# Optimization experiments

Measured on AMD Instinct MI355X. Metric: run time of the kernel, lower is better.

## Reference

```python
import jax, jax.numpy as jnp
import numpy as np

NEG_SLOPE = 0.2


def gat_layer(x, src, dst, W, a_src, a_dst, bias, num_nodes, concat):
    """PyG-style GATConv (eval mode, self-loops already included in src/dst).
    x: [N, F_in]; W: [F_in, H*C]; a_src, a_dst: [H, C]; bias: [H*C] or [C].
    """
    H, C = a_src.shape
    h = (x @ W).reshape(num_nodes, H, C)                    # [N,H,C]
    alpha_s = jnp.einsum('nhc,hc->nh', h, a_src)            # [N,H]
    alpha_d = jnp.einsum('nhc,hc->nh', h, a_dst)            # [N,H]
    e = alpha_s[src] + alpha_d[dst]                         # [E,H]
    e = jnp.where(e > 0, e, NEG_SLOPE * e)                  # LeakyReLU(0.2)
    # segment softmax over destination nodes (numerically stable)
    m = jax.ops.segment_max(e, dst, num_segments=num_nodes)  # [N,H]
    m = jnp.where(jnp.isfinite(m), m, 0.0)
    ex = jnp.exp(e - m[dst])                                # [E,H]
    s = jax.ops.segment_sum(ex, dst, num_segments=num_nodes)  # [N,H]
    alpha = ex / (s[dst] + 1e-16)                           # [E,H]
    msg = h[src] * alpha[:, :, None]                        # [E,H,C]
    out = jax.ops.segment_sum(msg, dst, num_segments=num_nodes)  # [N,H,C]
    if concat:
        out = out.reshape(num_nodes, H * C)
    else:
        out = out.mean(axis=1)
    return out + bias


def _forward(x, edge_index, W1, a_src1, a_dst1, b1, W2, a_src2, a_dst2, b2):
    N = x.shape[0]
    loops = jnp.arange(N, dtype=edge_index.dtype)
    src = jnp.concatenate([edge_index[0], loops])
    dst = jnp.concatenate([edge_index[1], loops])
    h = gat_layer(x, src, dst, W1, a_src1, a_dst1, b1, N, concat=True)
    h = jax.nn.relu(h)  # dropout inactive in eval
    h = gat_layer(h, src, dst, W2, a_src2, a_dst2, b2, N, concat=False)
    return jax.nn.log_softmax(h, axis=1)


def setup_inputs() -> dict:
    key = jax.random.key(0)
    ks = jax.random.split(key, 10)
    N, E, F_in, Hid, H1, F_out = 100000, 1600000, 128, 64, 2, 7
    x = jax.random.normal(ks[0], (N, F_in), dtype=jnp.float32)
    edge_index = jax.random.randint(ks[1], (2, E), 0, N, dtype=jnp.int64)
    s1 = 1.0 / np.sqrt(F_in)
    W1 = jax.random.uniform(ks[2], (F_in, H1 * Hid), jnp.float32, -s1, s1)
    a_src1 = jax.random.uniform(ks[3], (H1, Hid), jnp.float32, -s1, s1)
    a_dst1 = jax.random.uniform(ks[4], (H1, Hid), jnp.float32, -s1, s1)
    b1 = jnp.zeros((H1 * Hid,), jnp.float32)
    s2 = 1.0 / np.sqrt(H1 * Hid)
    W2 = jax.random.uniform(ks[5], (H1 * Hid, F_out), jnp.float32, -s2, s2)
    a_src2 = jax.random.uniform(ks[6], (1, F_out), jnp.float32, -s2, s2)
    a_dst2 = jax.random.uniform(ks[7], (1, F_out), jnp.float32, -s2, s2)
    b2 = jnp.zeros((F_out,), jnp.float32)
    return {"x": x, "edge_index": edge_index, "W1": W1, "a_src1": a_src1,
            "a_dst1": a_dst1, "b1": b1, "W2": W2, "a_src2": a_src2,
            "a_dst2": a_dst2, "b2": b2}


def reference(x, edge_index, W1, a_src1, a_dst1, b1, W2, a_src2, a_dst2, b2):
    return _forward(x, edge_index, W1, a_src1, a_dst1, b1, W2, a_src2, a_dst2, b2)
```

## Files before the change

kernel.cpp:

```cpp
#include <hip/hip_runtime.h>
#include <hip/hip_bf16.h>

#define F_IN 128
#define HC   128
#define C1   64
#define F_OUT 7
#define H2S  8
#define BSH  9
#define BSZ  512
#define BINCH 8192
#define BCAP 12288

typedef __attribute__((ext_vector_type(8))) short short8;
typedef __attribute__((ext_vector_type(4))) float f32x4;
typedef __attribute__((ext_vector_type(2))) float f32x2;

__device__ __forceinline__ ushort f2bf(float f) {
    uint u = __builtin_bit_cast(uint, f);
    u = (u + 0x7FFFu + ((u >> 16) & 1u)) >> 16;
    return (ushort)u;
}

__global__ __launch_bounds__(256) void k_bincvt(
    const int* __restrict__ ei, int E, int Etot, int NBIN,
    int* __restrict__ bcnt, uint* __restrict__ binned,
    const float* __restrict__ W1, ushort* __restrict__ Wsw,
    const float* __restrict__ W2, const float* __restrict__ b1,
    float* __restrict__ W2p, float* __restrict__ b1p)
{
    int b = blockIdx.x, t = threadIdx.x;
    if (b < NBIN) {
        __shared__ int hist[256];
        __shared__ int base[256];
        hist[t] = 0;
        __syncthreads();
        long c0 = (long)b * BINCH;
#pragma unroll
        for (int i = 0; i < BINCH / 256; ++i) {
            long e = c0 + t + i * 256;
            if (e < Etot) {
                int d = (e < E) ? ei[E + e] : (int)(e - E);
                atomicAdd(&hist[d >> BSH], 1);
            }
        }
        __syncthreads();
        base[t] = t * BCAP + ((hist[t] > 0) ? atomicAdd(&bcnt[t], hist[t]) : 0);
        __syncthreads();
#pragma unroll
        for (int i = 0; i < BINCH / 256; ++i) {
            long e = c0 + t + i * 256;
            if (e < Etot) {
                int s, d;
                if (e < E) { s = ei[e]; d = ei[E + e]; } else { s = (int)(e - E); d = s; }
                int bkt = d >> BSH;
                int pos = atomicAdd(&base[bkt], 1);
                if (pos < (bkt + 1) * BCAP)
                    binned[pos] = ((uint)s << BSH) | (uint)(d & (BSZ - 1));
            }
        }
    } else if (b < NBIN + 64) {
        int i = (b - NBIN) * 256 + t;
        int k = i >> 7, n = i & 127;
        float v = W1[k * HC + n];
        int idx = n * 128 + (((k & ~7) ^ ((n & 7) << 3)) | (k & 7));
        Wsw[idx] = f2bf(v);
    } else {
        for (int i = t; i < 128 * F_OUT; i += 256) {
            int p = i / F_OUT, o = i - p * F_OUT;
            int c = 16 * (p & 7) + (p >> 3);
            W2p[i] = W2[c * F_OUT + o];
        }
        if (t < 128) b1p[t] = b1[16 * (t & 7) + (t >> 3)];
    }
}

__global__ __launch_bounds__(256) void k_fillgemm(
    const uint* __restrict__ binned, const int* __restrict__ bcnt,
    int* __restrict__ rowptr, int* __restrict__ csr,
    const float* __restrict__ x, const ushort* __restrict__ Wsw,
    const float* __restrict__ a_src, const float* __restrict__ a_dst,
    unsigned char* __restrict__ h1p, float* __restrict__ as1, float* __restrict__ ad1,
    int N, int NB)
{
    __shared__ __align__(16) char smem[128 * 128 * 2];
    const int t = threadIdx.x;

    if ((int)blockIdx.x < NB) {
        int* deg = (int*)smem;
        int* cur = deg + BSZ;
        int* sc  = cur + BSZ;
        int b = blockIdx.x;
        int cv = (t < NB) ? min(bcnt[t], BCAP) : 0;
        sc[t] = cv;
        __syncthreads();
        for (int off = 1; off < 256; off <<= 1) {
            int u = (t >= off) ? sc[t - off] : 0;
            __syncthreads();
            sc[t] += u;
            __syncthreads();
        }
        int total = sc[255];
        int s0 = (b > 0) ? sc[b - 1] : 0;
        int cntb = min(bcnt[b], BCAP);
        __syncthreads();

        int n0 = b << BSH;
        int nn = N - n0; if (nn > BSZ) nn = BSZ;
        deg[t] = 0; deg[t + 256] = 0;
        __syncthreads();
        const uint* bb = binned + (size_t)b * BCAP;
        for (int i = t; i < cntb; i += 256)
            atomicAdd(&deg[bb[i] & (BSZ - 1)], 1);
        __syncthreads();
        int d0 = deg[2 * t], d1 = deg[2 * t + 1];
        int ts = d0 + d1;
        sc[t] = ts;
        __syncthreads();
        for (int off = 1; off < 256; off <<= 1) {
            int u = (t >= off) ? sc[t - off] : 0;
            __syncthreads();
            sc[t] += u;
            __syncthreads();
        }
        int ex = sc[t] - ts + s0;
        if (2 * t < nn)     { rowptr[n0 + 2 * t]     = ex;      cur[2 * t]     = ex; }
        if (2 * t + 1 < nn) { rowptr[n0 + 2 * t + 1] = ex + d0; cur[2 * t + 1] = ex + d0; }
        __syncthreads();
        for (int i = t; i < cntb; i += 256) {
            uint en = bb[i];
            int pos = atomicAdd(&cur[en & (BSZ - 1)], 1);
            csr[pos] = (int)(en >> BSH);
        }
        if (b == 0 && t == 0) rowptr[N] = total;
    } else {
        ushort* Bs = (ushort*)smem;
        const int w = t >> 6, l = t & 63;
        const int lr = l & 15, hi = l >> 4;
        const int n0 = (blockIdx.x - NB) * 64;

        {
            const uint4* src = (const uint4*)Wsw;
            uint4* dst = (uint4*)Bs;
#pragma unroll
            for (int it = 0; it < 8; ++it) dst[t + it * 256] = src[t + it * 256];
        }
        __syncthreads();

        f32x4 acc[8];
#pragma unroll
        for (int j = 0; j < 8; ++j) acc[j] = (f32x4){0.f, 0.f, 0.f, 0.f};

        int arow = n0 + w * 16 + lr;
        if (arow >= N) arow = N - 1;
        const float* aptr = x + (size_t)arow * F_IN + hi * 8;

#pragma unroll
        for (int kt = 0; kt < 4; ++kt) {
            float4 f0 = *(const float4*)(aptr + kt * 32);
            float4 f1 = *(const float4*)(aptr + kt * 32 + 4);
            short8 a;
            a[0] = (short)f2bf(f0.x); a[1] = (short)f2bf(f0.y);
            a[2] = (short)f2bf(f0.z); a[3] = (short)f2bf(f0.w);
            a[4] = (short)f2bf(f1.x); a[5] = (short)f2bf(f1.y);
            a[6] = (short)f2bf(f1.z); a[7] = (short)f2bf(f1.w);
#pragma unroll
            for (int j = 0; j < 8; ++j) {
                int rn = 16 * j + lr;
                int kidx = (kt * 32 + hi * 8) ^ ((rn & 7) << 3);
                short8 b = *(const short8*)(Bs + rn * 128 + kidx);
                acc[j] = __builtin_amdgcn_mfma_f32_16x16x32_bf16(a, b, acc[j], 0, 0, 0);
            }
        }

        float as_[8], ad_[8];
#pragma unroll
        for (int j = 0; j < 8; ++j) {
            int hd = j >> 2;
            int c = 16 * (j & 3) + lr;
            as_[j] = a_src[hd * C1 + c];
            ad_[j] = a_dst[hd * C1 + c];
        }
#pragma unroll
        for (int i = 0; i < 4; ++i) {
            int r = n0 + w * 16 + hi * 4 + i;
            float ps0 = 0, ps1 = 0, pd0 = 0, pd1 = 0;
#pragma unroll
            for (int j = 0; j < 4; ++j) { ps0 += acc[j][i] * as_[j]; pd0 += acc[j][i] * ad_[j]; }
#pragma unroll
            for (int j = 4; j < 8; ++j) { ps1 += acc[j][i] * as_[j]; pd1 += acc[j][i] * ad_[j]; }
#pragma unroll
            for (int off = 1; off <= 8; off <<= 1) {
                ps0 += __shfl_xor(ps0, off, 64);
                ps1 += __shfl_xor(ps1, off, 64);
                pd0 += __shfl_xor(pd0, off, 64);
                pd1 += __shfl_xor(pd1, off, 64);
            }
            if (r < N) {
                int lo = 0, hi2 = 0;
                lo  = __builtin_amdgcn_cvt_pk_fp8_f32(acc[0][i], acc[1][i], lo,  false);
                lo  = __builtin_amdgcn_cvt_pk_fp8_f32(acc[2][i], acc[3][i], lo,  true);
                hi2 = __builtin_amdgcn_cvt_pk_fp8_f32(acc[4][i], acc[5][i], hi2, false);
                hi2 = __builtin_amdgcn_cvt_pk_fp8_f32(acc[6][i], acc[7][i], hi2, true);
                *(uint2*)(h1p + (size_t)r * HC + lr * 8) = make_uint2((uint)lo, (uint)hi2);
                if (lr == 0) {
                    as1[r * 2 + 0] = ps0; as1[r * 2 + 1] = ps1;
                    ad1[r * 2 + 0] = pd0; ad1[r * 2 + 1] = pd1;
                }
            }
        }
    }
}

__global__ __launch_bounds__(256) void k_aggr1_l2(
    const int* __restrict__ rowptr, const int* __restrict__ csr_src,
    const float* __restrict__ as1, const float* __restrict__ ad1,
    const unsigned char* __restrict__ h1p, const float* __restrict__ b1p,
    const float* __restrict__ W2p, const float* __restrict__ a_src2,
    const float* __restrict__ a_dst2,
    float* __restrict__ h2p, float* __restrict__ as2, float* __restrict__ ad2,
    int N)
{
    int w = threadIdx.x >> 6, l = threadIdx.x & 63;
    int q = l >> 4, sl = l & 15;
    int n = blockIdx.x * 16 + w * 4 + q;
    if (n >= N) return;
    float2 advv = *(const float2*)&ad1[n * 2];
    int beg = rowptr[n], end = rowptr[n + 1];
    float ac[8];
#pragma unroll
    for (int c = 0; c < 8; ++c) ac[c] = 0.f;
    float s0 = 0.f, s1 = 0.f;

    int i = beg;
    for (; i + 4 <= end; i += 4) {
        int sv[4]; float2 Av[4]; uint2 Hv[4];
#pragma unroll
        for (int j = 0; j < 4; ++j) sv[j] = csr_src[i + j];
#pragma unroll
        for (int j = 0; j < 4; ++j) Av[j] = *(const float2*)&as1[sv[j] * 2];
#pragma unroll
        for (int j = 0; j < 4; ++j)
            Hv[j] = *(const uint2*)(h1p + (((size_t)(uint)sv[j]) << 7) + sl * 8);
#pragma unroll
        for (int j = 0; j < 4; ++j) {
            float a0 = Av[j].x + advv.x; a0 = a0 > 0.f ? a0 : 0.2f * a0;
            float a1 = Av[j].y + advv.y; a1 = a1 > 0.f ? a1 : 0.2f * a1;
            float e0 = __expf(a0), e1 = __expf(a1);
            s0 += e0; s1 += e1;
            f32x2 p01 = __builtin_amdgcn_cvt_pk_f32_fp8((int)Hv[j].x, false);
            f32x2 p23 = __builtin_amdgcn_cvt_pk_f32_fp8((int)Hv[j].x, true);
            f32x2 p45 = __builtin_amdgcn_cvt_pk_f32_fp8((int)Hv[j].y, false);
            f32x2 p67 = __builtin_amdgcn_cvt_pk_f32_fp8((int)Hv[j].y, true);
            ac[0] += e0 * p01[0]; ac[1] += e0 * p01[1];
            ac[2] += e0 * p23[0]; ac[3] += e0 * p23[1];
            ac[4] += e1 * p45[0]; ac[5] += e1 * p45[1];
            ac[6] += e1 * p67[0]; ac[7] += e1 * p67[1];
        }
    }
    for (; i < end; ++i) {
        int src = csr_src[i];
        float2 Av = *(const float2*)&as1[src * 2];
        uint2 hv = *(const uint2*)(h1p + (((size_t)(uint)src) << 7) + sl * 8);
        float a0 = Av.x + advv.x; a0 = a0 > 0.f ? a0 : 0.2f * a0;
        float a1 = Av.y + advv.y; a1 = a1 > 0.f ? a1 : 0.2f * a1;
        float e0 = __expf(a0), e1 = __expf(a1);
        s0 += e0; s1 += e1;
        f32x2 p01 = __builtin_amdgcn_cvt_pk_f32_fp8((int)hv.x, false);
        f32x2 p23 = __builtin_amdgcn_cvt_pk_f32_fp8((int)hv.x, true);
        f32x2 p45 = __builtin_amdgcn_cvt_pk_f32_fp8((int)hv.y, false);
        f32x2 p67 = __builtin_amdgcn_cvt_pk_f32_fp8((int)hv.y, true);
        ac[0] += e0 * p01[0]; ac[1] += e0 * p01[1];
        ac[2] += e0 * p23[0]; ac[3] += e0 * p23[1];
        ac[4] += e1 * p45[0]; ac[5] += e1 * p45[1];
        ac[6] += e1 * p67[0]; ac[7] += e1 * p67[1];
    }
    float inv0 = 1.f / (s0 + 1e-16f);
    float inv1 = 1.f / (s1 + 1e-16f);

    float4 bv0 = *(const float4*)&b1p[sl * 8];
    float4 bv1 = *(const float4*)&b1p[sl * 8 + 4];
    float v[8];
    v[0] = fmaxf(ac[0] * inv0 + bv0.x, 0.f);
    v[1] = fmaxf(ac[1] * inv0 + bv0.y, 0.f);
    v[2] = fmaxf(ac[2] * inv0 + bv0.z, 0.f);
    v[3] = fmaxf(ac[3] * inv0 + bv0.w, 0.f);
    v[4] = fmaxf(ac[4] * inv1 + bv1.x, 0.f);
    v[5] = fmaxf(ac[5] * inv1 + bv1.y, 0.f);
    v[6] = fmaxf(ac[6] * inv1 + bv1.z, 0.f);
    v[7] = fmaxf(ac[7] * inv1 + bv1.w, 0.f);

    float w2r[56];
    {
        const float4* wp = (const float4*)(W2p + sl * 56);
#pragma unroll
        for (int k = 0; k < 14; ++k) {
            float4 f = wp[k];
            w2r[4 * k + 0] = f.x; w2r[4 * k + 1] = f.y;
            w2r[4 * k + 2] = f.z; w2r[4 * k + 3] = f.w;
        }
    }
    float p[7];
#pragma unroll
    for (int j = 0; j < 7; ++j) p[j] = 0.f;
#pragma unroll
    for (int r = 0; r < 8; ++r)
#pragma unroll
        for (int j = 0; j < 7; ++j) p[j] += v[r] * w2r[r * 7 + j];
#pragma unroll
    for (int off = 1; off <= 8; off <<= 1)
#pragma unroll
        for (int j = 0; j < 7; ++j) p[j] += __shfl_xor(p[j], off, 64);

    if (sl == 0) {
        float asv = 0.f, adv2 = 0.f;
#pragma unroll
        for (int j = 0; j < 7; ++j) {
            h2p[(size_t)n * H2S + j] = p[j];
            asv += p[j] * a_src2[j];
            adv2 += p[j] * a_dst2[j];
        }
        h2p[(size_t)n * H2S + 7] = 0.f;
        as2[n] = asv; ad2[n] = adv2;
    }
}

__global__ __launch_bounds__(256) void k_aggr2ls(
    const int* __restrict__ rowptr, const int* __restrict__ csr_src,
    const float* __restrict__ as2, const float* __restrict__ ad2,
    const float* __restrict__ h2p, const float* __restrict__ b2,
    float* __restrict__ out, int N)
{
    int g = blockIdx.x * blockDim.x + threadIdx.x;
    int n = g >> 3, l = g & 7;
    if (n >= N) return;
    float adv = ad2[n];
    int beg = rowptr[n], end = rowptr[n + 1];
    float acc = 0.f, s = 0.f;
    int i = beg;
    for (; i + 4 <= end; i += 4) {
        int sv[4]; float Av[4], Hv[4];
#pragma unroll
        for (int j = 0; j < 4; ++j) sv[j] = csr_src[i + j];
#pragma unroll
        for (int j = 0; j < 4; ++j) Av[j] = as2[sv[j]];
#pragma unroll
        for (int j = 0; j < 4; ++j) Hv[j] = h2p[((size_t)(uint)sv[j]) * H2S + l];
#pragma unroll
        for (int j = 0; j < 4; ++j) {
            float a = Av[j] + adv;
            a = a > 0.f ? a : 0.2f * a;
            float e0 = __expf(a);
            s += e0;
            acc += e0 * Hv[j];
        }
    }
    for (; i < end; ++i) {
        int s0 = csr_src[i];
        float a = as2[s0] + adv;
        a = a > 0.f ? a : 0.2f * a;
        float e0 = __expf(a);
        s += e0;
        acc += e0 * h2p[((size_t)(uint)s0) * H2S + l];
    }
    float v = (l < 7) ? acc / (s + 1e-16f) + b2[l] : -1e30f;
    float m = v;
#pragma unroll
    for (int off = 1; off <= 4; off <<= 1)
        m = fmaxf(m, __shfl_xor(m, off, 8));
    float ex = (l < 7) ? __expf(v - m) : 0.f;
    float sum = ex;
#pragma unroll
    for (int off = 1; off <= 4; off <<= 1)
        sum += __shfl_xor(sum, off, 8);
    if (l < 7) out[(size_t)n * F_OUT + l] = v - m - __logf(sum);
}

extern "C" void kernel_launch(void* const* d_in, const int* in_sizes, int n_in,
                              void* d_out, int out_size, void* d_ws, size_t ws_size,
                              hipStream_t stream) {
    const float* x      = (const float*)d_in[0];
    const int*   ei     = (const int*)d_in[1];
    const float* W1     = (const float*)d_in[2];
    const float* a_src1 = (const float*)d_in[3];
    const float* a_dst1 = (const float*)d_in[4];
    const float* b1     = (const float*)d_in[5];
    const float* W2     = (const float*)d_in[6];
    const float* a_src2 = (const float*)d_in[7];
    const float* a_dst2 = (const float*)d_in[8];
    const float* b2     = (const float*)d_in[9];
    float* out = (float*)d_out;

    const int N    = in_sizes[0] / F_IN;
    const int E    = in_sizes[1] / 2;
    const int Etot = E + N;
    const int NB   = (N + BSZ - 1) >> BSH;
    const int NBIN = (Etot + BINCH - 1) / BINCH;

    char* ws = (char*)d_ws;
    size_t off = 0;
    auto A = [&](size_t bytes) -> void* {
        char* p = ws + off;
        off += (bytes + 255) & ~(size_t)255;
        return (void*)p;
    };
    ushort* Wsw    = (ushort*)A((size_t)128 * 128 * 2);
    float*  W2p    = (float*) A((size_t)128 * F_OUT * 4);
    float*  b1p    = (float*) A((size_t)128 * 4);
    unsigned char* h1p = (unsigned char*)A((size_t)N * HC);
    float*  as1    = (float*) A((size_t)N * 2 * 4);
    float*  ad1    = (float*) A((size_t)N * 2 * 4);
    int*    rowptr = (int*)   A((size_t)(N + 1) * 4);
    int*    csr    = (int*)   A((size_t)Etot * 4);
    int*    bcnt   = (int*)   A(256 * 4);
    uint*   binned = (uint*)  A((size_t)NB * BCAP * 4);
    float*  h2p    = (float*)binned;
    float*  as2    = (float*)((char*)binned + (((size_t)N * H2S * 4 + 255) & ~(size_t)255));
    float*  ad2    = (float*)((char*)as2 + (((size_t)N * 4 + 255) & ~(size_t)255));

    hipMemsetAsync(bcnt, 0, 256 * 4, stream);

    k_bincvt<<<NBIN + 65, 256, 0, stream>>>(ei, E, Etot, NBIN, bcnt, binned,
                                            W1, Wsw, W2, b1, W2p, b1p);
    k_fillgemm<<<NB + (N + 63) / 64, 256, 0, stream>>>(
        binned, bcnt, rowptr, csr,
        x, Wsw, a_src1, a_dst1, h1p, as1, ad1, N, NB);
    k_aggr1_l2<<<(N + 15) / 16, 256, 0, stream>>>(rowptr, csr, as1, ad1, h1p,
                                                  b1p, W2p, a_src2, a_dst2,
                                                  h2p, as2, ad2, N);
    k_aggr2ls<<<((size_t)N * 8 + 255) / 256, 256, 0, stream>>>(rowptr, csr, as2, ad2,
                                                               h2p, b2, out, N);
}
```

Before: 157.1 us.

## Permute h1 fp8 layout per head and halve threads in layer-2 aggregation

Changes the fp8 row layout of h1 so each lane's 8 bytes belong to a single head. Each lane in layer-1 aggregation then computes one exp and one attention load per edge instead of two, and accumulates with packed f32x2 math. W2 and b1 permutations are updated to match the new column order. Layer-2 aggregation now uses 4 lanes per node with float2 loads instead of 8 lanes, which cuts redundant csr and as2 loads and exp work but lowers thread-level parallelism.

```diff
diff --git a/kernel.cpp b/kernel.cpp
--- a/kernel.cpp
+++ b/kernel.cpp
@@ -19,6 +19,13 @@
     uint u = __builtin_bit_cast(uint, f);
     u = (u + 0x7FFFu + ((u >> 16) & 1u)) >> 16;
     return (ushort)u;
+}
+
+__device__ __forceinline__ int perm_col(int p_byte) {
+    int slp = p_byte >> 3, j = p_byte & 7;
+    int h = slp >> 3, sg = slp & 7;
+    int lr = 2 * sg + (j >> 2), jj = j & 3;
+    return 16 * (4 * h + jj) + lr;
 }
 
 __global__ __launch_bounds__(256) void k_bincvt(
@@ -67,10 +74,9 @@
     } else {
         for (int i = t; i < 128 * F_OUT; i += 256) {
             int p = i / F_OUT, o = i - p * F_OUT;
-            int c = 16 * (p & 7) + (p >> 3);
-            W2p[i] = W2[c * F_OUT + o];
-        }
-        if (t < 128) b1p[t] = b1[16 * (t & 7) + (t >> 3)];
+            W2p[i] = W2[perm_col(p) * F_OUT + o];
+        }
+        if (t < 128) b1p[t] = b1[perm_col(t)];
     }
 }
 
@@ -196,12 +202,13 @@
                 pd1 += __shfl_xor(pd1, off, 64);
             }
             if (r < N) {
-                int lo = 0, hi2 = 0;
-                lo  = __builtin_amdgcn_cvt_pk_fp8_f32(acc[0][i], acc[1][i], lo,  false);
-                lo  = __builtin_amdgcn_cvt_pk_fp8_f32(acc[2][i], acc[3][i], lo,  true);
-                hi2 = __builtin_amdgcn_cvt_pk_fp8_f32(acc[4][i], acc[5][i], hi2, false);
-                hi2 = __builtin_amdgcn_cvt_pk_fp8_f32(acc[6][i], acc[7][i], hi2, true);
-                *(uint2*)(h1p + (size_t)r * HC + lr * 8) = make_uint2((uint)lo, (uint)hi2);
+                int w0 = 0, w1 = 0;
+                w0 = __builtin_amdgcn_cvt_pk_fp8_f32(acc[0][i], acc[1][i], w0, false);
+                w0 = __builtin_amdgcn_cvt_pk_fp8_f32(acc[2][i], acc[3][i], w0, true);
+                w1 = __builtin_amdgcn_cvt_pk_fp8_f32(acc[4][i], acc[5][i], w1, false);
+                w1 = __builtin_amdgcn_cvt_pk_fp8_f32(acc[6][i], acc[7][i], w1, true);
+                *(uint*)(h1p + (size_t)r * HC + lr * 4)      = (uint)w0;
+                *(uint*)(h1p + (size_t)r * HC + 64 + lr * 4) = (uint)w1;
                 if (lr == 0) {
                     as1[r * 2 + 0] = ps0; as1[r * 2 + 1] = ps1;
                     ad1[r * 2 + 0] = pd0; ad1[r * 2 + 1] = pd1;
@@ -224,70 +231,60 @@
     int q = l >> 4, sl = l & 15;
     int n = blockIdx.x * 16 + w * 4 + q;
     if (n >= N) return;
-    float2 advv = *(const float2*)&ad1[n * 2];
+    const int h = sl >> 3;
+    const int boff = sl * 8;
+    float adv = ad1[n * 2 + h];
     int beg = rowptr[n], end = rowptr[n + 1];
-    float ac[8];
-#pragma unroll
-    for (int c = 0; c < 8; ++c) ac[c] = 0.f;
-    float s0 = 0.f, s1 = 0.f;
+    f32x2 ac01 = {0.f, 0.f}, ac23 = {0.f, 0.f}, ac45 = {0.f, 0.f}, ac67 = {0.f, 0.f};
+    float s = 0.f;
 
     int i = beg;
     for (; i + 4 <= end; i += 4) {
-        int sv[4]; float2 Av[4]; uint2 Hv[4];
+        int sv[4]; float Av[4]; uint2 Hv[4];
 #pragma unroll
         for (int j = 0; j < 4; ++j) sv[j] = csr_src[i + j];
 #pragma unroll
-        for (int j = 0; j < 4; ++j) Av[j] = *(const float2*)&as1[sv[j] * 2];
+        for (int j = 0; j < 4; ++j) Av[j] = as1[sv[j] * 2 + h];
 #pragma unroll
         for (int j = 0; j < 4; ++j)
-            Hv[j] = *(const uint2*)(h1p + (((size_t)(uint)sv[j]) << 7) + sl * 8);
+            Hv[j] = *(const uint2*)(h1p + (((size_t)(uint)sv[j]) << 7) + boff);
 #pragma unroll
         for (int j = 0; j < 4; ++j) {
-            float a0 = Av[j].x + advv.x; a0 = a0 > 0.f ? a0 : 0.2f * a0;
-            float a1 = Av[j].y + advv.y; a1 = a1 > 0.f ? a1 : 0.2f * a1;
-            float e0 = __expf(a0), e1 = __expf(a1);
-            s0 += e0; s1 += e1;
-            f32x2 p01 = __builtin_amdgcn_cvt_pk_f32_fp8((int)Hv[j].x, false);
-            f32x2 p23 = __builtin_amdgcn_cvt_pk_f32_fp8((int)Hv[j].x, true);
-            f32x2 p45 = __builtin_amdgcn_cvt_pk_f32_fp8((int)Hv[j].y, false);
-            f32x2 p67 = __builtin_amdgcn_cvt_pk_f32_fp8((int)Hv[j].y, true);
-            ac[0] += e0 * p01[0]; ac[1] += e0 * p01[1];
-            ac[2] += e0 * p23[0]; ac[3] += e0 * p23[1];
-            ac[4] += e1 * p45[0]; ac[5] += e1 * p45[1];
-            ac[6] += e1 * p67[0]; ac[7] += e1 * p67[1];
+            float a = Av[j] + adv; a = a > 0.f ? a : 0.2f * a;
+            float e = __expf(a);
+            s += e;
+            f32x2 ev = {e, e};
+            ac01 += ev * __builtin_amdgcn_cvt_pk_f32_fp8((int)Hv[j].x, false);
+            ac23 += ev * __builtin_amdgcn_cvt_pk_f32_fp8((int)Hv[j].x, true);
+            ac45 += ev * __builtin_amdgcn_cvt_pk_f32_fp8((int)Hv[j].y, false);
+            ac67 += ev * __builtin_amdgcn_cvt_pk_f32_fp8((int)Hv[j].y, true);
         }
     }
     for (; i < end; ++i) {
         int src = csr_src[i];
-        float2 Av = *(const float2*)&as1[src * 2];
-        uint2 hv = *(const uint2*)(h1p + (((size_t)(uint)src) << 7) + sl * 8);
-        float a0 = Av.x + advv.x; a0 = a0 > 0.f ? a0 : 0.2f * a0;
-        float a1 = Av.y + advv.y; a1 = a1 > 0.f ? a1 : 0.2f * a1;
-        float e0 = __expf(a0), e1 = __expf(a1);
-        s0 += e0; s1 += e1;
-        f32x2 p01 = __builtin_amdgcn_cvt_pk_f32_fp8((int)hv.x, false);
-        f32x2 p23 = __builtin_amdgcn_cvt_pk_f32_fp8((int)hv.x, true);
-        f32x2 p45 = __builtin_amdgcn_cvt_pk_f32_fp8((int)hv.y, false);
-        f32x2 p67 = __builtin_amdgcn_cvt_pk_f32_fp8((int)hv.y, true);
-        ac[0] += e0 * p01[0]; ac[1] += e0 * p01[1];
-        ac[2] += e0 * p23[0]; ac[3] += e0 * p23[1];
-        ac[4] += e1 * p45[0]; ac[5] += e1 * p45[1];
-        ac[6] += e1 * p67[0]; ac[7] += e1 * p67[1];
-    }
-    float inv0 = 1.f / (s0 + 1e-16f);
-    float inv1 = 1.f / (s1 + 1e-16f);
+        float a = as1[src * 2 + h] + adv; a = a > 0.f ? a : 0.2f * a;
+        float e = __expf(a);
+        s += e;
+        uint2 hv = *(const uint2*)(h1p + (((size_t)(uint)src) << 7) + boff);
+        f32x2 ev = {e, e};
+        ac01 += ev * __builtin_amdgcn_cvt_pk_f32_fp8((int)hv.x, false);
+        ac23 += ev * __builtin_amdgcn_cvt_pk_f32_fp8((int)hv.x, true);
+        ac45 += ev * __builtin_amdgcn_cvt_pk_f32_fp8((int)hv.y, false);
+        ac67 += ev * __builtin_amdgcn_cvt_pk_f32_fp8((int)hv.y, true);
+    }
+    float inv = 1.f / (s + 1e-16f);
 
     float4 bv0 = *(const float4*)&b1p[sl * 8];
     float4 bv1 = *(const float4*)&b1p[sl * 8 + 4];
     float v[8];
-    v[0] = fmaxf(ac[0] * inv0 + bv0.x, 0.f);
-    v[1] = fmaxf(ac[1] * inv0 + bv0.y, 0.f);
-    v[2] = fmaxf(ac[2] * inv0 + bv0.z, 0.f);
-    v[3] = fmaxf(ac[3] * inv0 + bv0.w, 0.f);
-    v[4] = fmaxf(ac[4] * inv1 + bv1.x, 0.f);
-    v[5] = fmaxf(ac[5] * inv1 + bv1.y, 0.f);
-    v[6] = fmaxf(ac[6] * inv1 + bv1.z, 0.f);
-    v[7] = fmaxf(ac[7] * inv1 + bv1.w, 0.f);
+    v[0] = fmaxf(ac01[0] * inv + bv0.x, 0.f);
+    v[1] = fmaxf(ac01[1] * inv + bv0.y, 0.f);
+    v[2] = fmaxf(ac23[0] * inv + bv0.z, 0.f);
+    v[3] = fmaxf(ac23[1] * inv + bv0.w, 0.f);
+    v[4] = fmaxf(ac45[0] * inv + bv1.x, 0.f);
+    v[5] = fmaxf(ac45[1] * inv + bv1.y, 0.f);
+    v[6] = fmaxf(ac67[0] * inv + bv1.z, 0.f);
+    v[7] = fmaxf(ac67[1] * inv + bv1.w, 0.f);
 
     float w2r[56];
     {
@@ -331,48 +328,58 @@
     float* __restrict__ out, int N)
 {
     int g = blockIdx.x * blockDim.x + threadIdx.x;
-    int n = g >> 3, l = g & 7;
+    int n = g >> 2, l = g & 3;
     if (n >= N) return;
     float adv = ad2[n];
     int beg = rowptr[n], end = rowptr[n + 1];
-    float acc = 0.f, s = 0.f;
+    f32x2 acc = {0.f, 0.f};
+    float s = 0.f;
     int i = beg;
     for (; i + 4 <= end; i += 4) {
-        int sv[4]; float Av[4], Hv[4];
+        int sv[4]; float Av[4]; float2 Hv[4];
 #pragma unroll
         for (int j = 0; j < 4; ++j) sv[j] = csr_src[i + j];
 #pragma unroll
         for (int j = 0; j < 4; ++j) Av[j] = as2[sv[j]];
 #pragma unroll
-        for (int j = 0; j < 4; ++j) Hv[j] = h2p[((size_t)(uint)sv[j]) * H2S + l];
+        for (int j = 0; j < 4; ++j)
+            Hv[j] = *(const float2*)(h2p + ((size_t)(uint)sv[j]) * H2S + 2 * l);
 #pragma unroll
         for (int j = 0; j < 4; ++j) {
             float a = Av[j] + adv;
             a = a > 0.f ? a : 0.2f * a;
-            float e0 = __expf(a);
-            s += e0;
-            acc += e0 * Hv[j];
+            float e = __expf(a);
+            s += e;
+            f32x2 ev = {e, e};
+            f32x2 hv = {Hv[j].x, Hv[j].y};
+            acc += ev * hv;
         }
     }
     for (; i < end; ++i) {
         int s0 = csr_src[i];
         float a = as2[s0] + adv;
         a = a > 0.f ? a : 0.2f * a;
-        float e0 = __expf(a);
-        s += e0;
-        acc += e0 * h2p[((size_t)(uint)s0) * H2S + l];
-    }
-    float v = (l < 7) ? acc / (s + 1e-16f) + b2[l] : -1e30f;
-    float m = v;
-#pragma unroll
-    for (int off = 1; off <= 4; off <<= 1)
-        m = fmaxf(m, __shfl_xor(m, off, 8));
-    float ex = (l < 7) ? __expf(v - m) : 0.f;
-    float sum = ex;
-#pragma unroll
-    for (int off = 1; off <= 4; off <<= 1)
-        sum += __shfl_xor(sum, off, 8);
-    if (l < 7) out[(size_t)n * F_OUT + l] = v - m - __logf(sum);
+        float e = __expf(a);
+        s += e;
+        float2 hv2 = *(const float2*)(h2p + ((size_t)(uint)s0) * H2S + 2 * l);
+        f32x2 ev = {e, e};
+        f32x2 hv = {hv2.x, hv2.y};
+        acc += ev * hv;
+    }
+    float invs = 1.f / (s + 1e-16f);
+    float va = acc[0] * invs + b2[2 * l];
+    float vb = (2 * l + 1 < 7) ? acc[1] * invs + b2[2 * l + 1] : -1e30f;
+    float m = fmaxf(va, vb);
+#pragma unroll
+    for (int off = 1; off <= 2; off <<= 1)
+        m = fmaxf(m, __shfl_xor(m, off, 4));
+    float ex = __expf(va - m) + ((2 * l + 1 < 7) ? __expf(vb - m) : 0.f);
+#pragma unroll
+    for (int off = 1; off <= 2; off <<= 1)
+        ex += __shfl_xor(ex, off, 4);
+    float lg = __logf(ex);
+    out[(size_t)n * F_OUT + 2 * l] = va - m - lg;
+    if (2 * l + 1 < 7) out[(size_t)n * F_OUT + 2 * l + 1] = vb - m - lg;
 }
 
 extern "C" void kernel_launch(void* const* d_in, const int* in_sizes, int n_in,
@@ -427,6 +434,6 @@
     k_aggr1_l2<<<(N + 15) / 16, 256, 0, stream>>>(rowptr, csr, as1, ad1, h1p,
                                                   b1p, W2p, a_src2, a_dst2,
                                                   h2p, as2, ad2, N);
-    k_aggr2ls<<<((size_t)N * 8 + 255) / 256, 256, 0, stream>>>(rowptr, csr, as2, ad2,
+    k_aggr2ls<<<((size_t)N * 4 + 255) / 256, 256, 0, stream>>>(rowptr, csr, as2, ad2,
                                                                h2p, b2, out, N);
 }
```

Measured after the change: 147.5 us. 1.06x faster.
